# Optimization experiments

Measured on AMD Instinct MI355X. Metric: run time of the kernel, lower is better.

The kernel has to match this reference:

```python
import jax, jax.numpy as jnp
import numpy as np

N, M, E, DIM, H = 50000, 50000, 640000, 128, 8
DH = DIM // H
EPS = 1e-5

def _prelu(x, alpha):
    return jnp.where(x >= 0, x, alpha * x)

def setup_inputs() -> dict:
    key0 = jax.random.key(0)
    ks = jax.random.split(key0, 12)
    s = 1.0 / np.sqrt(DIM)
    return {
        "query": jax.random.normal(ks[0], (N, DIM), jnp.float32),
        "key": jax.random.normal(ks[1], (M, DIM), jnp.float32),
        "value": jax.random.normal(ks[2], (M, DIM), jnp.float32),
        "query_idx": jax.random.randint(ks[3], (E,), 0, N),
        "key_idx": jax.random.randint(ks[4], (E,), 0, M),
        "Wq": jax.random.normal(ks[5], (DIM, DIM), jnp.float32) * s,
        "bq": jnp.zeros((DIM,), jnp.float32),
        "Wk": jax.random.normal(ks[6], (DIM, DIM), jnp.float32) * s,
        "bk": jnp.zeros((DIM,), jnp.float32),
        "Wv": jax.random.normal(ks[7], (DIM, DIM), jnp.float32) * s,
        "bv": jnp.zeros((DIM,), jnp.float32),
        "Wp": jax.random.normal(ks[8], (DIM, DIM), jnp.float32) * s,
        "bp": jnp.zeros((DIM,), jnp.float32),
        "a": jax.random.normal(ks[9], (1, H, DH), jnp.float32) * 0.1,
        "alpha": jnp.full((1,), 0.25, jnp.float32),
        "gamma": jnp.ones((DIM,), jnp.float32),
        "beta": jnp.zeros((DIM,), jnp.float32),
    }

def reference(query, key, value, query_idx, key_idx, Wq, bq, Wk, bk, Wv, bv, Wp, bp, a, alpha, gamma, beta):
    n = query.shape[0]
    # projections (node-level, then gather per edge; linear commutes with gather)
    Qq = query @ Wq + bq            # [N, DIM]
    Kq = query @ Wk + bk            # [N, DIM] (self-attn key)
    Kk = key @ Wk + bk              # [M, DIM]
    Vq = query @ Wv + bv            # [N, DIM]
    Vv = value @ Wv + bv            # [M, DIM]
    # self-attention score per query node: [N, H, 1]
    attn_qq = (a * _prelu(Qq + Kq, alpha).reshape(n, H, DH)).sum(-1, keepdims=True)
    # per-edge additive attention score: [E, H, 1]
    e_feat = _prelu(Qq[query_idx] + Kk[key_idx], alpha)
    attn_e = (a * e_feat.reshape(-1, H, DH)).sum(-1, keepdims=True)
    # stable softmax over irregular query groups (include self)
    max_attn = jax.lax.stop_gradient(attn_qq.at[query_idx].max(attn_e))
    exp_qq = jnp.exp(attn_qq - max_attn)                 # [N, H, 1]
    exp_e = jnp.exp(attn_e - max_attn[query_idx])        # [E, H, 1]
    denom = exp_qq.at[query_idx].add(exp_e)              # [N, H, 1]
    denom = jnp.where(denom == 0, 1.0, denom)
    # weighted value scatter-sum (value_idx == key_idx)
    msg = exp_qq * Vq.reshape(n, H, DH)
    msg = msg.at[query_idx].add(exp_e * Vv[key_idx].reshape(-1, H, DH))
    out = (msg / denom).reshape(n, DIM) @ Wp + bp
    res = query + out
    mu = res.mean(-1, keepdims=True)
    var = res.var(-1, keepdims=True)
    return gamma * (res - mu) / jnp.sqrt(var + EPS) + beta
```

## Files before the change

### kernel.cpp

```cpp
#include <hip/hip_runtime.h>
#include <math.h>

#define DIM 128
#define NH 8
#define LN_EPS 1e-5f
#define NEGINF -3.0e38f

using bf16x8 = __attribute__((ext_vector_type(8))) short;
using f32x4  = __attribute__((ext_vector_type(4))) float;

__device__ __forceinline__ float prelu_f(float x, float al) { return x >= 0.f ? x : al * x; }

__device__ __forceinline__ short f2bf(float f) {
    unsigned u = __float_as_uint(f);
    unsigned r = (u + 0x7fffu + ((u >> 16) & 1u)) >> 16;
    return (short)r;
}
__device__ __forceinline__ float bflo(unsigned u) { return __uint_as_float(u << 16); }
__device__ __forceinline__ float bfhi(unsigned u) { return __uint_as_float(u & 0xffff0000u); }

__device__ __forceinline__ unsigned cvt_pk_bf16(float lo, float hi) {
    unsigned r;
    asm("v_cvt_pk_bf16_f32 %0, %1, %2" : "=v"(r) : "v"(lo), "v"(hi));
    return r;
}

__device__ __forceinline__ float swz_xor1(float x) {
    return __int_as_float(__builtin_amdgcn_ds_swizzle(__float_as_int(x), 0x041F));
}
__device__ __forceinline__ float swz_xor2(float x) {
    return __int_as_float(__builtin_amdgcn_ds_swizzle(__float_as_int(x), 0x081F));
}
__device__ __forceinline__ float swz_xor4(float x) {
    return __int_as_float(__builtin_amdgcn_ds_swizzle(__float_as_int(x), 0x101F));
}
__device__ __forceinline__ float swz_xor8(float x) {
    return __int_as_float(__builtin_amdgcn_ds_swizzle(__float_as_int(x), 0x201F));
}
__device__ __forceinline__ float swz_xor16(float x) {
    return __int_as_float(__builtin_amdgcn_ds_swizzle(__float_as_int(x), 0x401F));
}
__device__ __forceinline__ float swz_xor32(float x) {
    return __shfl_xor(x, 32);
}

__global__ __launch_bounds__(256) void setup_kernel(
    const float* __restrict__ W0, const float* __restrict__ W1,
    const float* __restrict__ W2, const float* __restrict__ W3,
    short* __restrict__ P0, short* __restrict__ P1,
    short* __restrict__ P2, short* __restrict__ P3,
    const int* __restrict__ qidx, int* __restrict__ counts, int E)
{
    if (blockIdx.x < 32) {
        const int id = blockIdx.x * 256 + threadIdx.x;
        const int mat = id >> 11;
        const int rem = id & 2047;
        const int ks = rem >> 9;
        const int ct = (rem >> 6) & 7;
        const int lane = rem & 63;
        const int lr = lane & 15, lg = lane >> 4;
        const float* W = mat == 0 ? W0 : mat == 1 ? W1 : mat == 2 ? W2 : W3;
        short* P = mat == 0 ? P0 : mat == 1 ? P1 : mat == 2 ? P2 : P3;
        short v[8];
        #pragma unroll
        for (int r = 0; r < 8; ++r)
            v[r] = f2bf(W[(ks * 32 + lg * 8 + r) * DIM + ct * 16 + lr]);
        *(bf16x8*)&P[(size_t)((ks * 8 + ct) * 64 + lane) * 8] = *(bf16x8*)v;
    } else {
        const int b = blockIdx.x - 32;
        for (int e = b * 256 + threadIdx.x; e < E; e += 1024 * 256)
            atomicAdd(&counts[qidx[e]], 1);
    }
}

__global__ __launch_bounds__(256) void proj_all_mfma(
    const float* __restrict__ query,
    const float* __restrict__ key, const float* __restrict__ value,
    const short* __restrict__ Wqp, const short* __restrict__ Wkp, const short* __restrict__ Wvp,
    const float* __restrict__ bq, const float* __restrict__ bk, const float* __restrict__ bv,
    const float* __restrict__ avec, const float* __restrict__ alpha_p,
    short* __restrict__ QV16, float* __restrict__ attnqq,
    short* __restrict__ KV16, int N, int M, int nb)
{
    __shared__ float lds[4][16][130];
    const int wid = threadIdx.x >> 6, lane = threadIdx.x & 63;
    const int lr = lane & 15, lg = lane >> 4;
    const int cl = lane * 2;

    if ((int)blockIdx.x < nb) {
        const int row0 = (blockIdx.x * 4 + wid) * 16;
        if (row0 >= N) return;
        bf16x8 afrag[4];
        const int arow = row0 + lr;
        const bool rowok = arow < N;
        #pragma unroll
        for (int ks = 0; ks < 4; ++ks) {
            float t[8] = {0.f,0.f,0.f,0.f,0.f,0.f,0.f,0.f};
            if (rowok) {
                *(float4*)&t[0] = *(const float4*)&query[(size_t)arow * DIM + ks * 32 + lg * 8];
                *(float4*)&t[4] = *(const float4*)&query[(size_t)arow * DIM + ks * 32 + lg * 8 + 4];
            }
            bf16x8 a;
            #pragma unroll
            for (int j = 0; j < 8; ++j) a[j] = f2bf(t[j]);
            afrag[ks] = a;
        }

        f32x4 accQ[8], accK[8], accV[8];
        #pragma unroll
        for (int ct = 0; ct < 8; ++ct) { accQ[ct] = (f32x4)0.f; accK[ct] = (f32x4)0.f; accV[ct] = (f32x4)0.f; }
        #pragma unroll
        for (int ks = 0; ks < 4; ++ks) {
            #pragma unroll
            for (int ct = 0; ct < 8; ++ct) {
                const size_t bo = (size_t)((ks * 8 + ct) * 64 + lane) * 8;
                const bf16x8 bq_ = *(const bf16x8*)&Wqp[bo];
                const bf16x8 bk_ = *(const bf16x8*)&Wkp[bo];
                const bf16x8 bv_ = *(const bf16x8*)&Wvp[bo];
                accQ[ct] = __builtin_amdgcn_mfma_f32_16x16x32_bf16(afrag[ks], bq_, accQ[ct], 0, 0, 0);
                accK[ct] = __builtin_amdgcn_mfma_f32_16x16x32_bf16(afrag[ks], bk_, accK[ct], 0, 0, 0);
                accV[ct] = __builtin_amdgcn_mfma_f32_16x16x32_bf16(afrag[ks], bv_, accV[ct], 0, 0, 0);
            }
        }

        const float al = alpha_p[0];
        #pragma unroll
        for (int ct = 0; ct < 8; ++ct) {
            const int col = ct * 16 + lr;
            const float bqv = bq[col], bkv = bk[col], av = avec[col];
            #pragma unroll
            for (int r = 0; r < 4; ++r) {
                const int grow = row0 + lg * 4 + r;
                const float qv = accQ[ct][r] + bqv;
                const float kv = accK[ct][r] + bkv;
                lds[wid][lg * 4 + r][col] = qv;
                float part = av * prelu_f(qv + kv, al);
                part += swz_xor1(part);
                part += swz_xor2(part);
                part += swz_xor4(part);
                part += swz_xor8(part);
                if (lr == 0 && grow < N) attnqq[(size_t)grow * NH + ct] = part;
            }
        }
        #pragma unroll
        for (int rr = 0; rr < 16; ++rr) {
            const int grow = row0 + rr;
            if (grow < N) {
                const float2 t = *(const float2*)&lds[wid][rr][cl];
                *(unsigned*)&QV16[(size_t)grow * 256 + cl] = cvt_pk_bf16(t.x, t.y);
            }
        }
        #pragma unroll
        for (int ct = 0; ct < 8; ++ct) {
            const int col = ct * 16 + lr;
            const float bvv = bv[col];
            #pragma unroll
            for (int r = 0; r < 4; ++r)
                lds[wid][lg * 4 + r][col] = accV[ct][r] + bvv;
        }
        #pragma unroll
        for (int rr = 0; rr < 16; ++rr) {
            const int grow = row0 + rr;
            if (grow < N) {
                const float2 t = *(const float2*)&lds[wid][rr][cl];
                *(unsigned*)&QV16[(size_t)grow * 256 + 128 + cl] = cvt_pk_bf16(t.x, t.y);
            }
        }
    } else {
        const int row0 = (((int)blockIdx.x - nb) * 4 + wid) * 16;
        if (row0 >= M) return;
        bf16x8 afK[4], afV[4];
        const int arow = row0 + lr;
        const bool rowok = arow < M;
        #pragma unroll
        for (int ks = 0; ks < 4; ++ks) {
            float tk[8] = {0.f,0.f,0.f,0.f,0.f,0.f,0.f,0.f};
            float tv[8] = {0.f,0.f,0.f,0.f,0.f,0.f,0.f,0.f};
            if (rowok) {
                *(float4*)&tk[0] = *(const float4*)&key[(size_t)arow * DIM + ks * 32 + lg * 8];
                *(float4*)&tk[4] = *(const float4*)&key[(size_t)arow * DIM + ks * 32 + lg * 8 + 4];
                *(float4*)&tv[0] = *(const float4*)&value[(size_t)arow * DIM + ks * 32 + lg * 8];
                *(float4*)&tv[4] = *(const float4*)&value[(size_t)arow * DIM + ks * 32 + lg * 8 + 4];
            }
            bf16x8 a, b;
            #pragma unroll
            for (int j = 0; j < 8; ++j) { a[j] = f2bf(tk[j]); b[j] = f2bf(tv[j]); }
            afK[ks] = a; afV[ks] = b;
        }

        f32x4 accK[8], accV[8];
        #pragma unroll
        for (int ct = 0; ct < 8; ++ct) { accK[ct] = (f32x4)0.f; accV[ct] = (f32x4)0.f; }
        #pragma unroll
        for (int ks = 0; ks < 4; ++ks) {
            #pragma unroll
            for (int ct = 0; ct < 8; ++ct) {
                const size_t bo = (size_t)((ks * 8 + ct) * 64 + lane) * 8;
                const bf16x8 bk_ = *(const bf16x8*)&Wkp[bo];
                const bf16x8 bv_ = *(const bf16x8*)&Wvp[bo];
                accK[ct] = __builtin_amdgcn_mfma_f32_16x16x32_bf16(afK[ks], bk_, accK[ct], 0, 0, 0);
                accV[ct] = __builtin_amdgcn_mfma_f32_16x16x32_bf16(afV[ks], bv_, accV[ct], 0, 0, 0);
            }
        }

        #pragma unroll
        for (int ct = 0; ct < 8; ++ct) {
            const int col = ct * 16 + lr;
            const float bkv = bk[col];
            #pragma unroll
            for (int r = 0; r < 4; ++r)
                lds[wid][lg * 4 + r][col] = accK[ct][r] + bkv;
        }
        #pragma unroll
        for (int rr = 0; rr < 16; ++rr) {
            const int grow = row0 + rr;
            if (grow < M) {
                const float2 t = *(const float2*)&lds[wid][rr][cl];
                *(unsigned*)&KV16[(size_t)grow * 256 + cl] = cvt_pk_bf16(t.x, t.y);
            }
        }
        #pragma unroll
        for (int ct = 0; ct < 8; ++ct) {
            const int col = ct * 16 + lr;
            const float bvv = bv[col];
            #pragma unroll
            for (int r = 0; r < 4; ++r)
                lds[wid][lg * 4 + r][col] = accV[ct][r] + bvv;
        }
        #pragma unroll
        for (int rr = 0; rr < 16; ++rr) {
            const int grow = row0 + rr;
            if (grow < M) {
                const float2 t = *(const float2*)&lds[wid][rr][cl];
                *(unsigned*)&KV16[(size_t)grow * 256 + 128 + cl] = cvt_pk_bf16(t.x, t.y);
            }
        }
    }
}

__global__ __launch_bounds__(256) void scan1_kernel(const int* __restrict__ counts,
                                                    int* __restrict__ bsum, int N)
{
    __shared__ int sh[256];
    int i = blockIdx.x * 256 + threadIdx.x;
    sh[threadIdx.x] = (i < N) ? counts[i] : 0;
    __syncthreads();
    #pragma unroll
    for (int off = 128; off; off >>= 1) {
        if (threadIdx.x < off) sh[threadIdx.x] += sh[threadIdx.x + off];
        __syncthreads();
    }
    if (threadIdx.x == 0) bsum[blockIdx.x] = sh[0];
}

__global__ __launch_bounds__(256) void scan2_kernel(const int* __restrict__ bsum,
                                                    int* __restrict__ boff, int B)
{
    int t = threadIdx.x;
    if (B > 256) {
        if (t == 0) { int run = 0; for (int i = 0; i < B; ++i) { int v = bsum[i]; boff[i] = run; run += v; } }
        return;
    }
    __shared__ int sh[256];
    int v = (t < B) ? bsum[t] : 0;
    sh[t] = v;
    __syncthreads();
    for (int off = 1; off < 256; off <<= 1) {
        int x = (t >= off) ? sh[t - off] : 0;
        __syncthreads();
        sh[t] += x;
        __syncthreads();
    }
    if (t < B) boff[t] = sh[t] - v;
}

__global__ __launch_bounds__(256) void scan3_kernel(const int* __restrict__ counts,
                                                    const int* __restrict__ boff,
                                                    int* __restrict__ offsets,
                                                    int* __restrict__ cursor,
                                                    int N, int E)
{
    __shared__ int sh[256];
    int t = threadIdx.x;
    int i = blockIdx.x * 256 + t;
    int v = (i < N) ? counts[i] : 0;
    sh[t] = v;
    __syncthreads();
    for (int off = 1; off < 256; off <<= 1) {
        int x = (t >= off) ? sh[t - off] : 0;
        __syncthreads();
        sh[t] += x;
        __syncthreads();
    }
    int base = boff[blockIdx.x];
    if (i < N) {
        int o = base + sh[t] - v;
        offsets[i] = o;
        cursor[i] = o;
    }
    if (i == 0) offsets[N] = E;
}

__global__ void fill_kernel(const int* __restrict__ qidx, const int* __restrict__ kidx,
                            int* __restrict__ cursor, int* __restrict__ ksorted, int E)
{
    for (int e = blockIdx.x * blockDim.x + threadIdx.x; e < E; e += gridDim.x * blockDim.x) {
        int q = qidx[e];
        int pos = atomicAdd(&cursor[q], 1);
        ksorted[pos] = kidx[e];
    }
}

__global__ __launch_bounds__(256) void edge_agg_kernel(
    const short* __restrict__ QV16, const float* __restrict__ attnqq,
    const short* __restrict__ KV16,
    const int* __restrict__ ksorted, const int* __restrict__ offsets,
    const float* __restrict__ avec, const float* __restrict__ alpha_p,
    short* __restrict__ msgn16, int N)
{
    const int wid = threadIdx.x >> 6;
    const int lane = threadIdx.x & 63;
    const int n = blockIdx.x * 4 + wid;
    if (n >= N) return;

    const int h = lane & 7;
    const int e = lane >> 3;
    const float al = alpha_p[0];

    float c1[16], c2[16];
    {
        const float s1 = (1.f + al) * 0.5f, s2 = (1.f - al) * 0.5f;
        #pragma unroll
        for (int j = 0; j < 4; ++j) {
            const float4 a4 = *(const float4*)&avec[h * 16 + j * 4];
            c1[j*4+0] = a4.x * s1; c2[j*4+0] = a4.x * s2;
            c1[j*4+1] = a4.y * s1; c2[j*4+1] = a4.y * s2;
            c1[j*4+2] = a4.z * s1; c2[j*4+2] = a4.z * s2;
            c1[j*4+3] = a4.w * s1; c2[j*4+3] = a4.w * s2;
        }
    }

    const size_t qb = (size_t)n * 256 + h * 16;
    float q[16];
    {
        const uint4 lo = *(const uint4*)&QV16[qb];
        const uint4 hi = *(const uint4*)&QV16[qb + 8];
        const unsigned qd[8] = {lo.x, lo.y, lo.z, lo.w, hi.x, hi.y, hi.z, hi.w};
        #pragma unroll
        for (int j = 0; j < 8; ++j) { q[2*j] = bflo(qd[j]); q[2*j+1] = bfhi(qd[j]); }
    }

    float acc[16];
    float den;
    if (e == 0) {
        const uint4 lo = *(const uint4*)&QV16[qb + 128];
        const uint4 hi = *(const uint4*)&QV16[qb + 136];
        const unsigned vd[8] = {lo.x, lo.y, lo.z, lo.w, hi.x, hi.y, hi.z, hi.w};
        #pragma unroll
        for (int j = 0; j < 8; ++j) { acc[2*j] = bflo(vd[j]); acc[2*j+1] = bfhi(vd[j]); }
        den = 1.f;
    } else {
        #pragma unroll
        for (int d = 0; d < 16; ++d) acc[d] = 0.f;
        den = 0.f;
    }

    float m = attnqq[(size_t)n * NH + h];
    const int p0 = offsets[n], p1 = offsets[n + 1];
    bool div = false;

    int idx = p0 + e;
    bool valid = idx < p1;
    int ki = valid ? ksorted[idx] : 0;

    for (int base = p0; base < p1; base += 8) {
        const int cki = ki;
        const bool cval = valid;
        const int nidx = base + 8 + e;
        valid = nidx < p1;
        ki = valid ? ksorted[nidx] : 0;

        const size_t kb = (size_t)cki * 256 + h * 16;
        const uint4 klo = *(const uint4*)&KV16[kb];
        const uint4 khi = *(const uint4*)&KV16[kb + 8];
        const uint4 vlo = *(const uint4*)&KV16[kb + 128];
        const uint4 vhi = *(const uint4*)&KV16[kb + 136];
        const unsigned kd[8] = {klo.x, klo.y, klo.z, klo.w, khi.x, khi.y, khi.z, khi.w};
        const unsigned vd[8] = {vlo.x, vlo.y, vlo.z, vlo.w, vhi.x, vhi.y, vhi.z, vhi.w};

        float sA = 0.f, sB = 0.f;
        #pragma unroll
        for (int j = 0; j < 8; ++j) {
            const float x0 = q[2*j]   + bflo(kd[j]);
            const float x1 = q[2*j+1] + bfhi(kd[j]);
            sA = fmaf(c1[2*j],   x0, fmaf(c2[2*j],   __builtin_fabsf(x0), sA));
            sB = fmaf(c1[2*j+1], x1, fmaf(c2[2*j+1], __builtin_fabsf(x1), sB));
        }
        const float s = cval ? (sA + sB) : NEGINF;
        const float d_ = s - m;

        if (__any(d_ > 8.f)) {
            div = true;
            const float nm = fmaxf(m, s);
            const float c = __expf(m - nm);
            const float w = __expf(s - nm);
            den = den * c + w;
            #pragma unroll
            for (int j = 0; j < 8; ++j) {
                acc[2*j]   = fmaf(acc[2*j],   c, w * bflo(vd[j]));
                acc[2*j+1] = fmaf(acc[2*j+1], c, w * bfhi(vd[j]));
            }
            m = nm;
        } else {
            const float w = __expf(d_);
            den += w;
            #pragma unroll
            for (int j = 0; j < 8; ++j) {
                acc[2*j]   = fmaf(w, bflo(vd[j]), acc[2*j]);
                acc[2*j+1] = fmaf(w, bfhi(vd[j]), acc[2*j+1]);
            }
        }
    }

    #define MERGE_ROUND(SWZ)                                    \
        {                                                       \
            const float m2 = SWZ(m);                            \
            const float den2 = SWZ(den);                        \
            const float nm = fmaxf(m, m2);                      \
            const float ca = __expf(m - nm);                    \
            const float cb = __expf(m2 - nm);                   \
            den = den * ca + den2 * cb;                         \
            _Pragma("unroll")                                   \
            for (int d = 0; d < 16; ++d)                        \
                acc[d] = acc[d] * ca + SWZ(acc[d]) * cb;        \
            m = nm;                                             \
        }
    #define SUM_ROUND(SWZ)                                      \
        {                                                       \
            den += SWZ(den);                                    \
            _Pragma("unroll")                                   \
            for (int d = 0; d < 16; ++d) acc[d] += SWZ(acc[d]); \
        }

    if (div) {
        MERGE_ROUND(swz_xor8);
        MERGE_ROUND(swz_xor16);
        MERGE_ROUND(swz_xor32);
    } else {
        SUM_ROUND(swz_xor8);
        SUM_ROUND(swz_xor16);
        SUM_ROUND(swz_xor32);
    }
    #undef MERGE_ROUND
    #undef SUM_ROUND

    if (e == 0) {
        const float inv = 1.f / den;
        unsigned u[8];
        #pragma unroll
        for (int j = 0; j < 8; ++j)
            u[j] = cvt_pk_bf16(acc[2*j] * inv, acc[2*j+1] * inv);
        *(uint4*)&msgn16[(size_t)n * DIM + h * 16]     = make_uint4(u[0], u[1], u[2], u[3]);
        *(uint4*)&msgn16[(size_t)n * DIM + h * 16 + 8] = make_uint4(u[4], u[5], u[6], u[7]);
    }
}

__global__ __launch_bounds__(256) void out_ln_mfma(
    const short* __restrict__ msgn16, const short* __restrict__ Wpp,
    const float* __restrict__ bp, const float* __restrict__ query,
    const float* __restrict__ gamma, const float* __restrict__ beta,
    float* __restrict__ out, int N)
{
    __shared__ float ys[64][130];
    const int wid = threadIdx.x >> 6, lane = threadIdx.x & 63;
    const int rowbase = blockIdx.x * 64;
    const int row0 = rowbase + wid * 16;
    const int lr = lane & 15, lg = lane >> 4;

    if (row0 < N) {
        bf16x8 afrag[4];
        const int arow = row0 + lr;
        const bool rowok = arow < N;
        #pragma unroll
        for (int ks = 0; ks < 4; ++ks) {
            if (rowok)
                afrag[ks] = *(const bf16x8*)&msgn16[(size_t)arow * DIM + ks * 32 + lg * 8];
            else {
                bf16x8 z;
                #pragma unroll
                for (int j = 0; j < 8; ++j) z[j] = 0;
                afrag[ks] = z;
            }
        }
        f32x4 acc[8];
        #pragma unroll
        for (int ct = 0; ct < 8; ++ct) acc[ct] = (f32x4)0.f;
        #pragma unroll
        for (int ks = 0; ks < 4; ++ks) {
            #pragma unroll
            for (int ct = 0; ct < 8; ++ct) {
                const size_t bo = (size_t)((ks * 8 + ct) * 64 + lane) * 8;
                const bf16x8 b_ = *(const bf16x8*)&Wpp[bo];
                acc[ct] = __builtin_amdgcn_mfma_f32_16x16x32_bf16(afrag[ks], b_, acc[ct], 0, 0, 0);
            }
        }
        #pragma unroll
        for (int ct = 0; ct < 8; ++ct) {
            const int col = ct * 16 + lr;
            const float bpv = bp[col];
            #pragma unroll
            for (int r = 0; r < 4; ++r)
                ys[wid * 16 + lg * 4 + r][col] = acc[ct][r] + bpv;
        }
    }
    __syncthreads();

    for (int rr = 0; rr < 16; ++rr) {
        const int r = wid * 16 + rr;
        const int grow = rowbase + r;
        if (grow >= N) break;
        const float y1 = ys[r][lane], y2 = ys[r][lane + 64];
        const float q1 = query[(size_t)grow * DIM + lane];
        const float q2 = query[(size_t)grow * DIM + lane + 64];
        const float r1 = y1 + q1, r2 = y2 + q2;
        float s = r1 + r2;
        float ss = r1 * r1 + r2 * r2;
        #pragma unroll
        for (int off = 32; off; off >>= 1) {
            s += __shfl_xor(s, off);
            ss += __shfl_xor(ss, off);
        }
        const float mu = s * (1.f / DIM);
        const float var = ss * (1.f / DIM) - mu * mu;
        const float rstd = rsqrtf(var + LN_EPS);
        out[(size_t)grow * DIM + lane] = gamma[lane] * (r1 - mu) * rstd + beta[lane];
        out[(size_t)grow * DIM + lane + 64] = gamma[lane + 64] * (r2 - mu) * rstd + beta[lane + 64];
    }
}

extern "C" void kernel_launch(void* const* d_in, const int* in_sizes, int n_in,
                              void* d_out, int out_size, void* d_ws, size_t ws_size,
                              hipStream_t stream) {
    const float* query = (const float*)d_in[0];
    const float* key   = (const float*)d_in[1];
    const float* value = (const float*)d_in[2];
    const int* query_idx = (const int*)d_in[3];
    const int* key_idx   = (const int*)d_in[4];
    const float* Wq = (const float*)d_in[5];
    const float* bq = (const float*)d_in[6];
    const float* Wk = (const float*)d_in[7];
    const float* bk = (const float*)d_in[8];
    const float* Wv = (const float*)d_in[9];
    const float* bv = (const float*)d_in[10];
    const float* Wp = (const float*)d_in[11];
    const float* bp = (const float*)d_in[12];
    const float* avec  = (const float*)d_in[13];
    const float* alpha = (const float*)d_in[14];
    const float* gamma = (const float*)d_in[15];
    const float* beta  = (const float*)d_in[16];
    float* out = (float*)d_out;

    const int N = in_sizes[0] / DIM;
    const int M = in_sizes[1] / DIM;
    const int E = in_sizes[3];

    float* f = (float*)d_ws;
    float* attnqq = f;  f += (size_t)N * NH;
    short* sp = (short*)f;
    short* QV16 = sp;   sp += (size_t)N * 256;
    short* KV16 = sp;   sp += (size_t)M * 256;
    short* msgn16 = sp; sp += (size_t)N * DIM;
    short* Wqp = sp;    sp += DIM * DIM;
    short* Wkp = sp;    sp += DIM * DIM;
    short* Wvp = sp;    sp += DIM * DIM;
    short* Wpp = sp;    sp += DIM * DIM;
    int* ip = (int*)(((size_t)sp + 15) & ~(size_t)15);
    int* counts  = ip;  ip += N;
    int* offsets = ip;  ip += N + 1;
    int* cursor  = ip;  ip += N;
    int* bsum    = ip;  ip += 4096;
    int* boff    = ip;  ip += 4096;
    int* ksorted = ip;  ip += E;

    const int B = (N + 255) / 256;
    const int nb = (N + 63) / 64;
    const int mb = (M + 63) / 64;

    hipMemsetAsync(counts, 0, (size_t)N * sizeof(int), stream);

    setup_kernel<<<1056, 256, 0, stream>>>(Wq, Wk, Wv, Wp, Wqp, Wkp, Wvp, Wpp,
                                           query_idx, counts, E);

    scan1_kernel<<<B, 256, 0, stream>>>(counts, bsum, N);
    scan2_kernel<<<1, 256, 0, stream>>>(bsum, boff, B);
    scan3_kernel<<<B, 256, 0, stream>>>(counts, boff, offsets, cursor, N, E);
    fill_kernel<<<1024, 256, 0, stream>>>(query_idx, key_idx, cursor, ksorted, E);

    proj_all_mfma<<<nb + mb, 256, 0, stream>>>(
        query, key, value, Wqp, Wkp, Wvp, bq, bk, bv, avec, alpha,
        QV16, attnqq, KV16, N, M, nb);

    edge_agg_kernel<<<(N + 3) / 4, 256, 0, stream>>>(
        QV16, attnqq, KV16, ksorted, offsets, avec, alpha, msgn16, N);

    out_ln_mfma<<<(N + 63) / 64, 256, 0, stream>>>(
        msgn16, Wpp, bp, query, gamma, beta, out, N);
}
```

Measured before the change: 224.4 us.

## Restructure projection GEMMs per column tile to cut register pressure

The projection kernels now loop over column tiles on the outside with a single accumulator per output, instead of holding all 8 (or 24) accumulator tiles live. Bias and epilogue run per tile. Packing to bf16 now happens before the LDS staging, using a lane-pair swizzle, and the K and V input fragments are loaded in separate phases. The output projection kernel gets the same loop interchange. The aim is lower VGPR usage, higher occupancy and less LDS traffic, at the cost of less MFMA interleaving and serialized tile loops (unroll 1), which may expose latency.

Measured after the change: 206.7 us. 7.9% less time.

```diff
diff --git a/kernel.cpp b/kernel.cpp
--- a/kernel.cpp
+++ b/kernel.cpp
@@ -82,17 +82,18 @@
     short* __restrict__ QV16, float* __restrict__ attnqq,
     short* __restrict__ KV16, int N, int M, int nb)
 {
-    __shared__ float lds[4][16][130];
+    __shared__ unsigned lds[4][16][66];
     const int wid = threadIdx.x >> 6, lane = threadIdx.x & 63;
     const int lr = lane & 15, lg = lane >> 4;
-    const int cl = lane * 2;
+    const bool evenlane = (lane & 1) == 0;
 
     if ((int)blockIdx.x < nb) {
-        const int row0 = (blockIdx.x * 4 + wid) * 16;
+        const int row0 = ((int)blockIdx.x * 4 + wid) * 16;
         if (row0 >= N) return;
-        bf16x8 afrag[4];
         const int arow = row0 + lr;
         const bool rowok = arow < N;
+
+        bf16x8 afrag[4];
         #pragma unroll
         for (int ks = 0; ks < 4; ++ks) {
             float t[8] = {0.f,0.f,0.f,0.f,0.f,0.f,0.f,0.f};
@@ -100,139 +101,157 @@
                 *(float4*)&t[0] = *(const float4*)&query[(size_t)arow * DIM + ks * 32 + lg * 8];
                 *(float4*)&t[4] = *(const float4*)&query[(size_t)arow * DIM + ks * 32 + lg * 8 + 4];
             }
-            bf16x8 a;
-            #pragma unroll
-            for (int j = 0; j < 8; ++j) a[j] = f2bf(t[j]);
-            afrag[ks] = a;
-        }
-
-        f32x4 accQ[8], accK[8], accV[8];
-        #pragma unroll
-        for (int ct = 0; ct < 8; ++ct) { accQ[ct] = (f32x4)0.f; accK[ct] = (f32x4)0.f; accV[ct] = (f32x4)0.f; }
-        #pragma unroll
-        for (int ks = 0; ks < 4; ++ks) {
-            #pragma unroll
-            for (int ct = 0; ct < 8; ++ct) {
+            union { bf16x8 v; unsigned u[4]; } a;
+            a.u[0] = cvt_pk_bf16(t[0], t[1]);
+            a.u[1] = cvt_pk_bf16(t[2], t[3]);
+            a.u[2] = cvt_pk_bf16(t[4], t[5]);
+            a.u[3] = cvt_pk_bf16(t[6], t[7]);
+            afrag[ks] = a.v;
+        }
+        const float al = alpha_p[0];
+        unsigned* qvout = (unsigned*)QV16;
+
+        #pragma unroll 1
+        for (int ct = 0; ct < 8; ++ct) {
+            f32x4 aq = (f32x4)0.f, ak = (f32x4)0.f;
+            #pragma unroll
+            for (int ks = 0; ks < 4; ++ks) {
                 const size_t bo = (size_t)((ks * 8 + ct) * 64 + lane) * 8;
-                const bf16x8 bq_ = *(const bf16x8*)&Wqp[bo];
-                const bf16x8 bk_ = *(const bf16x8*)&Wkp[bo];
-                const bf16x8 bv_ = *(const bf16x8*)&Wvp[bo];
-                accQ[ct] = __builtin_amdgcn_mfma_f32_16x16x32_bf16(afrag[ks], bq_, accQ[ct], 0, 0, 0);
-                accK[ct] = __builtin_amdgcn_mfma_f32_16x16x32_bf16(afrag[ks], bk_, accK[ct], 0, 0, 0);
-                accV[ct] = __builtin_amdgcn_mfma_f32_16x16x32_bf16(afrag[ks], bv_, accV[ct], 0, 0, 0);
-            }
-        }
-
-        const float al = alpha_p[0];
-        #pragma unroll
-        for (int ct = 0; ct < 8; ++ct) {
+                aq = __builtin_amdgcn_mfma_f32_16x16x32_bf16(afrag[ks], *(const bf16x8*)&Wqp[bo], aq, 0, 0, 0);
+                ak = __builtin_amdgcn_mfma_f32_16x16x32_bf16(afrag[ks], *(const bf16x8*)&Wkp[bo], ak, 0, 0, 0);
+            }
             const int col = ct * 16 + lr;
             const float bqv = bq[col], bkv = bk[col], av = avec[col];
             #pragma unroll
             for (int r = 0; r < 4; ++r) {
-                const int grow = row0 + lg * 4 + r;
-                const float qv = accQ[ct][r] + bqv;
-                const float kv = accK[ct][r] + bkv;
-                lds[wid][lg * 4 + r][col] = qv;
+                const int row = lg * 4 + r;
+                const float qv = aq[r] + bqv;
+                const float kv = ak[r] + bkv;
                 float part = av * prelu_f(qv + kv, al);
                 part += swz_xor1(part);
                 part += swz_xor2(part);
                 part += swz_xor4(part);
                 part += swz_xor8(part);
+                const int grow = row0 + row;
                 if (lr == 0 && grow < N) attnqq[(size_t)grow * NH + ct] = part;
+                const float qn = swz_xor1(qv);
+                if (evenlane) lds[wid][row][ct * 8 + (lr >> 1)] = cvt_pk_bf16(qv, qn);
             }
         }
         #pragma unroll
         for (int rr = 0; rr < 16; ++rr) {
             const int grow = row0 + rr;
-            if (grow < N) {
-                const float2 t = *(const float2*)&lds[wid][rr][cl];
-                *(unsigned*)&QV16[(size_t)grow * 256 + cl] = cvt_pk_bf16(t.x, t.y);
-            }
-        }
-        #pragma unroll
+            if (grow < N) qvout[(size_t)grow * 128 + lane] = lds[wid][rr][lane];
+        }
+
+        #pragma unroll 1
         for (int ct = 0; ct < 8; ++ct) {
+            f32x4 acv = (f32x4)0.f;
+            #pragma unroll
+            for (int ks = 0; ks < 4; ++ks) {
+                const size_t bo = (size_t)((ks * 8 + ct) * 64 + lane) * 8;
+                acv = __builtin_amdgcn_mfma_f32_16x16x32_bf16(afrag[ks], *(const bf16x8*)&Wvp[bo], acv, 0, 0, 0);
+            }
             const int col = ct * 16 + lr;
             const float bvv = bv[col];
             #pragma unroll
-            for (int r = 0; r < 4; ++r)
-                lds[wid][lg * 4 + r][col] = accV[ct][r] + bvv;
+            for (int r = 0; r < 4; ++r) {
+                const int row = lg * 4 + r;
+                const float vv = acv[r] + bvv;
+                const float vn = swz_xor1(vv);
+                if (evenlane) lds[wid][row][ct * 8 + (lr >> 1)] = cvt_pk_bf16(vv, vn);
+            }
         }
         #pragma unroll
         for (int rr = 0; rr < 16; ++rr) {
             const int grow = row0 + rr;
-            if (grow < N) {
-                const float2 t = *(const float2*)&lds[wid][rr][cl];
-                *(unsigned*)&QV16[(size_t)grow * 256 + 128 + cl] = cvt_pk_bf16(t.x, t.y);
-            }
+            if (grow < N) qvout[(size_t)grow * 128 + 64 + lane] = lds[wid][rr][lane];
         }
     } else {
         const int row0 = (((int)blockIdx.x - nb) * 4 + wid) * 16;
         if (row0 >= M) return;
-        bf16x8 afK[4], afV[4];
         const int arow = row0 + lr;
         const bool rowok = arow < M;
-        #pragma unroll
-        for (int ks = 0; ks < 4; ++ks) {
-            float tk[8] = {0.f,0.f,0.f,0.f,0.f,0.f,0.f,0.f};
-            float tv[8] = {0.f,0.f,0.f,0.f,0.f,0.f,0.f,0.f};
-            if (rowok) {
-                *(float4*)&tk[0] = *(const float4*)&key[(size_t)arow * DIM + ks * 32 + lg * 8];
-                *(float4*)&tk[4] = *(const float4*)&key[(size_t)arow * DIM + ks * 32 + lg * 8 + 4];
-                *(float4*)&tv[0] = *(const float4*)&value[(size_t)arow * DIM + ks * 32 + lg * 8];
-                *(float4*)&tv[4] = *(const float4*)&value[(size_t)arow * DIM + ks * 32 + lg * 8 + 4];
-            }
-            bf16x8 a, b;
-            #pragma unroll
-            for (int j = 0; j < 8; ++j) { a[j] = f2bf(tk[j]); b[j] = f2bf(tv[j]); }
-            afK[ks] = a; afV[ks] = b;
-        }
-
-        f32x4 accK[8], accV[8];
-        #pragma unroll
-        for (int ct = 0; ct < 8; ++ct) { accK[ct] = (f32x4)0.f; accV[ct] = (f32x4)0.f; }
-        #pragma unroll
-        for (int ks = 0; ks < 4; ++ks) {
-            #pragma unroll
+        unsigned* kvout = (unsigned*)KV16;
+
+        {
+            bf16x8 afK[4];
+            #pragma unroll
+            for (int ks = 0; ks < 4; ++ks) {
+                float t[8] = {0.f,0.f,0.f,0.f,0.f,0.f,0.f,0.f};
+                if (rowok) {
+                    *(float4*)&t[0] = *(const float4*)&key[(size_t)arow * DIM + ks * 32 + lg * 8];
+                    *(float4*)&t[4] = *(const float4*)&key[(size_t)arow * DIM + ks * 32 + lg * 8 + 4];
+                }
+                union { bf16x8 v; unsigned u[4]; } a;
+                a.u[0] = cvt_pk_bf16(t[0], t[1]);
+                a.u[1] = cvt_pk_bf16(t[2], t[3]);
+                a.u[2] = cvt_pk_bf16(t[4], t[5]);
+                a.u[3] = cvt_pk_bf16(t[6], t[7]);
+                afK[ks] = a.v;
+            }
+            #pragma unroll 1
             for (int ct = 0; ct < 8; ++ct) {
-                const size_t bo = (size_t)((ks * 8 + ct) * 64 + lane) * 8;
-                const bf16x8 bk_ = *(const bf16x8*)&Wkp[bo];
-                const bf16x8 bv_ = *(const bf16x8*)&Wvp[bo];
-                accK[ct] = __builtin_amdgcn_mfma_f32_16x16x32_bf16(afK[ks], bk_, accK[ct], 0, 0, 0);
-                accV[ct] = __builtin_amdgcn_mfma_f32_16x16x32_bf16(afV[ks], bv_, accV[ct], 0, 0, 0);
-            }
-        }
-
-        #pragma unroll
-        for (int ct = 0; ct < 8; ++ct) {
-            const int col = ct * 16 + lr;
-            const float bkv = bk[col];
-            #pragma unroll
-            for (int r = 0; r < 4; ++r)
-                lds[wid][lg * 4 + r][col] = accK[ct][r] + bkv;
-        }
-        #pragma unroll
-        for (int rr = 0; rr < 16; ++rr) {
-            const int grow = row0 + rr;
-            if (grow < M) {
-                const float2 t = *(const float2*)&lds[wid][rr][cl];
-                *(unsigned*)&KV16[(size_t)grow * 256 + cl] = cvt_pk_bf16(t.x, t.y);
-            }
-        }
-        #pragma unroll
-        for (int ct = 0; ct < 8; ++ct) {
-            const int col = ct * 16 + lr;
-            const float bvv = bv[col];
-            #pragma unroll
-            for (int r = 0; r < 4; ++r)
-                lds[wid][lg * 4 + r][col] = accV[ct][r] + bvv;
-        }
-        #pragma unroll
-        for (int rr = 0; rr < 16; ++rr) {
-            const int grow = row0 + rr;
-            if (grow < M) {
-                const float2 t = *(const float2*)&lds[wid][rr][cl];
-                *(unsigned*)&KV16[(size_t)grow * 256 + 128 + cl] = cvt_pk_bf16(t.x, t.y);
+                f32x4 ack = (f32x4)0.f;
+                #pragma unroll
+                for (int ks = 0; ks < 4; ++ks) {
+                    const size_t bo = (size_t)((ks * 8 + ct) * 64 + lane) * 8;
+                    ack = __builtin_amdgcn_mfma_f32_16x16x32_bf16(afK[ks], *(const bf16x8*)&Wkp[bo], ack, 0, 0, 0);
+                }
+                const int col = ct * 16 + lr;
+                const float bkv = bk[col];
+                #pragma unroll
+                for (int r = 0; r < 4; ++r) {
+                    const int row = lg * 4 + r;
+                    const float kv = ack[r] + bkv;
+                    const float kn = swz_xor1(kv);
+                    if (evenlane) lds[wid][row][ct * 8 + (lr >> 1)] = cvt_pk_bf16(kv, kn);
+                }
+            }
+            #pragma unroll
+            for (int rr = 0; rr < 16; ++rr) {
+                const int grow = row0 + rr;
+                if (grow < M) kvout[(size_t)grow * 128 + lane] = lds[wid][rr][lane];
+            }
+        }
+        {
+            bf16x8 afV[4];
+            #pragma unroll
+            for (int ks = 0; ks < 4; ++ks) {
+                float t[8] = {0.f,0.f,0.f,0.f,0.f,0.f,0.f,0.f};
+                if (rowok) {
+                    *(float4*)&t[0] = *(const float4*)&value[(size_t)arow * DIM + ks * 32 + lg * 8];
+                    *(float4*)&t[4] = *(const float4*)&value[(size_t)arow * DIM + ks * 32 + lg * 8 + 4];
+                }
+                union { bf16x8 v; unsigned u[4]; } a;
+                a.u[0] = cvt_pk_bf16(t[0], t[1]);
+                a.u[1] = cvt_pk_bf16(t[2], t[3]);
+                a.u[2] = cvt_pk_bf16(t[4], t[5]);
+                a.u[3] = cvt_pk_bf16(t[6], t[7]);
+                afV[ks] = a.v;
+            }
+            #pragma unroll 1
+            for (int ct = 0; ct < 8; ++ct) {
+                f32x4 acv = (f32x4)0.f;
+                #pragma unroll
+                for (int ks = 0; ks < 4; ++ks) {
+                    const size_t bo = (size_t)((ks * 8 + ct) * 64 + lane) * 8;
+                    acv = __builtin_amdgcn_mfma_f32_16x16x32_bf16(afV[ks], *(const bf16x8*)&Wvp[bo], acv, 0, 0, 0);
+                }
+                const int col = ct * 16 + lr;
+                const float bvv = bv[col];
+                #pragma unroll
+                for (int r = 0; r < 4; ++r) {
+                    const int row = lg * 4 + r;
+                    const float vv = acv[r] + bvv;
+                    const float vn = swz_xor1(vv);
+                    if (evenlane) lds[wid][row][ct * 8 + (lr >> 1)] = cvt_pk_bf16(vv, vn);
+                }
+            }
+            #pragma unroll
+            for (int rr = 0; rr < 16; ++rr) {
+                const int grow = row0 + rr;
+                if (grow < M) kvout[(size_t)grow * 128 + 64 + lane] = lds[wid][rr][lane];
             }
         }
     }
@@ -492,25 +511,19 @@
                 afrag[ks] = z;
             }
         }
-        f32x4 acc[8];
-        #pragma unroll
-        for (int ct = 0; ct < 8; ++ct) acc[ct] = (f32x4)0.f;
-        #pragma unroll
-        for (int ks = 0; ks < 4; ++ks) {
-            #pragma unroll
-            for (int ct = 0; ct < 8; ++ct) {
+        #pragma unroll 1
+        for (int ct = 0; ct < 8; ++ct) {
+            f32x4 acc = (f32x4)0.f;
+            #pragma unroll
+            for (int ks = 0; ks < 4; ++ks) {
                 const size_t bo = (size_t)((ks * 8 + ct) * 64 + lane) * 8;
-                const bf16x8 b_ = *(const bf16x8*)&Wpp[bo];
-                acc[ct] = __builtin_amdgcn_mfma_f32_16x16x32_bf16(afrag[ks], b_, acc[ct], 0, 0, 0);
-            }
-        }
-        #pragma unroll
-        for (int ct = 0; ct < 8; ++ct) {
+                acc = __builtin_amdgcn_mfma_f32_16x16x32_bf16(afrag[ks], *(const bf16x8*)&Wpp[bo], acc, 0, 0, 0);
+            }
             const int col = ct * 16 + lr;
             const float bpv = bp[col];
             #pragma unroll
             for (int r = 0; r < 4; ++r)
-                ys[wid * 16 + lg * 4 + r][col] = acc[ct][r] + bpv;
+                ys[wid * 16 + lg * 4 + r][col] = acc[r] + bpv;
         }
     }
     __syncthreads();
```
